# Kernel tuning notes

Hardware: AMD Instinct MI355X
Metric: run time of the kernel (lower is better)

Reference implementation:

```python
import jax, jax.numpy as jnp
import numpy as np

HEAD_DIM = 128
PROJ_DIM = 64


def setup_inputs() -> dict:
    key = jax.random.key(0)
    kq, kk, kv, kr = jax.random.split(key, 4)
    B, H, NQ, NKV = 1, 16, 2048, 4096
    Q = jax.random.normal(kq, (B, H, NQ, HEAD_DIM), dtype=jnp.float32)
    K = jax.random.normal(kk, (B, H, NKV, HEAD_DIM), dtype=jnp.float32)
    V = jax.random.normal(kv, (B, H, NKV, HEAD_DIM), dtype=jnp.float32)
    # R ~ N(0,1) / sqrt(proj_dim), as in the torch __init__
    R = jax.random.normal(kr, (HEAD_DIM, PROJ_DIM), dtype=jnp.float32) / (PROJ_DIM ** 0.5)
    return {"Q": Q, "K": K, "V": V, "R": R}


def reference(Q, K, V, R):
    proj_dim = R.shape[-1]
    scale = 1.0 / (proj_dim ** 0.5)
    # Project Q and K into the random-projection space: [B,H,N,proj_dim]
    Q_proj = jnp.einsum('bhnd,dp->bhnp', Q, R)
    K_proj = jnp.einsum('bhmd,dp->bhmp', K, R)
    # scores: [B,H,NQ,NKV]
    scores = jnp.einsum('bhnp,bhmp->bhnm', Q_proj, K_proj) * scale
    weights = jax.nn.softmax(scores, axis=-1)
    # output: [B,H,NQ,head_dim]
    return jnp.einsum('bhnm,bhmd->bhnd', weights, V)
```

## Files before the change

kernel.cpp:

```cpp
#include <hip/hip_runtime.h>

#define HEADS 16
#define NQ    2048
#define NKV   4096
#define DH    128
#define PDIM  64

typedef __bf16 bf16_t;
typedef bf16_t bf16x8 __attribute__((ext_vector_type(8)));
typedef float  f32x4  __attribute__((ext_vector_type(4)));

__global__ __launch_bounds__(256) void proj_kernel(
    const float* __restrict__ Q, const float* __restrict__ K,
    const float* __restrict__ R, bf16_t* __restrict__ Qp, bf16_t* __restrict__ Kp)
{
  const int tid  = threadIdx.x;
  const int wave = tid >> 6, lane = tid & 63;
  const int n16  = lane & 15, quad = lane >> 4;

  bf16x8 bfr[4][4];
#pragma unroll
  for (int nt = 0; nt < 4; ++nt) {
    const int n = nt * 16 + n16;
#pragma unroll
    for (int kk = 0; kk < 4; ++kk) {
      const int k0 = kk * 32 + quad * 8;
      bf16x8 b;
#pragma unroll
      for (int j = 0; j < 8; ++j) b[j] = (bf16_t)R[(k0 + j) * PDIM + n];
      bfr[nt][kk] = b;
    }
  }

  const long rowblock = (long)blockIdx.x * 256 + wave * 64;
  const long qrows = (long)HEADS * NQ;

#pragma unroll 1
  for (int t = 0; t < 4; ++t) {
    const long r0 = rowblock + t * 16;
    const float* X; bf16_t* Y; float scale; long xrow;
    if (r0 < qrows) { X = Q; Y = Qp; scale = 0.18033688011112042f; xrow = r0; }
    else            { X = K; Y = Kp; scale = 1.0f;                 xrow = r0 - qrows; }

    const float* xp = X + (xrow + n16) * DH;
    bf16x8 a[4];
#pragma unroll
    for (int kk = 0; kk < 4; ++kk) {
      const int k0 = kk * 32 + quad * 8;
      f32x4 x0 = *(const f32x4*)(xp + k0);
      f32x4 x1 = *(const f32x4*)(xp + k0 + 4);
      bf16x8 av;
#pragma unroll
      for (int j = 0; j < 4; ++j) { av[j] = (bf16_t)(x0[j] * scale); av[4 + j] = (bf16_t)(x1[j] * scale); }
      a[kk] = av;
    }
#pragma unroll
    for (int nt = 0; nt < 4; ++nt) {
      f32x4 acc = {0.f, 0.f, 0.f, 0.f};
#pragma unroll
      for (int kk = 0; kk < 4; ++kk)
        acc = __builtin_amdgcn_mfma_f32_16x16x32_bf16(a[kk], bfr[nt][kk], acc, 0, 0, 0);
#pragma unroll
      for (int r = 0; r < 4; ++r)
        Y[(xrow + quad * 4 + r) * PDIM + nt * 16 + n16] = (bf16_t)acc[r];
    }
  }
}

__global__ __launch_bounds__(256) void vtrans_kernel(
    const float* __restrict__ V, bf16_t* __restrict__ Vt)
{
  __shared__ float sF[64 * 129];
  const int tid = threadIdx.x;
  const int h = blockIdx.y, jt = blockIdx.x;
  const float* vp = V + ((long)h * NKV + jt * 64) * DH;
#pragma unroll
  for (int rep = 0; rep < 8; ++rep) {
    const int slot = tid + rep * 256;
    const int j = slot >> 5, c4 = (slot & 31) * 4;
    f32x4 v = *(const f32x4*)(vp + j * DH + c4);
    float* dst = &sF[j * 129 + c4];
    dst[0] = v[0]; dst[1] = v[1]; dst[2] = v[2]; dst[3] = v[3];
  }
  __syncthreads();
  bf16_t* op = Vt + (long)h * DH * NKV + jt * 64;
#pragma unroll
  for (int rep = 0; rep < 4; ++rep) {
    const int slot = tid + rep * 256;
    const int d = slot >> 3, j8 = (slot & 7) * 8;
    bf16x8 w;
#pragma unroll
    for (int jj = 0; jj < 8; ++jj) w[jj] = (bf16_t)sF[(j8 + jj) * 129 + d];
    *(bf16x8*)(op + (long)d * NKV + j8) = w;
  }
}

__global__ __launch_bounds__(128, 2) void flash_kernel(
    const bf16_t* __restrict__ Qp, const bf16_t* __restrict__ Kp,
    const bf16_t* __restrict__ Vt, float* __restrict__ Out)
{
  const int tid  = threadIdx.x;
  const int wave = tid >> 6, lane = tid & 63;
  const int n16  = lane & 15, quad = lane >> 4;

  const int h  = blockIdx.x & 15;
  const int qt = blockIdx.x >> 4;

  __shared__ bf16_t sK[64 * 72];
  __shared__ bf16_t sV[128 * 72];
  __shared__ bf16_t sP[2][32 * 72];

  bf16x8 aq[2][2];
#pragma unroll
  for (int mh = 0; mh < 2; ++mh) {
    const bf16_t* qrow = Qp + ((long)h * NQ + qt * 64 + wave * 32 + mh * 16 + n16) * PDIM;
    aq[mh][0] = *(const bf16x8*)(qrow + quad * 8);
    aq[mh][1] = *(const bf16x8*)(qrow + 32 + quad * 8);
  }

  f32x4 o[2][8];
  float rsum[2][4];
  const f32x4 zero = {0.f, 0.f, 0.f, 0.f};
#pragma unroll
  for (int mh = 0; mh < 2; ++mh) {
#pragma unroll
    for (int d = 0; d < 8; ++d) o[mh][d] = zero;
#pragma unroll
    for (int r = 0; r < 4; ++r) rsum[mh][r] = 0.f;
  }

  const bf16_t* kpH = Kp + (long)h * NKV * PDIM;
  const bf16_t* vtH = Vt + (long)h * DH * NKV;

  for (int t = 0; t < NKV / 64; ++t) {
    __syncthreads();
    {
      const bf16_t* src = kpH + t * (64 * PDIM);
#pragma unroll
      for (int rep = 0; rep < 4; ++rep) {
        const int slot = tid + rep * 128;
        const int row = slot >> 3, c8 = (slot & 7) * 8;
        *(bf16x8*)(&sK[row * 72 + c8]) = *(const bf16x8*)(src + row * 64 + c8);
      }
      const bf16_t* vsrc = vtH + t * 64;
#pragma unroll
      for (int rep = 0; rep < 8; ++rep) {
        const int slot = tid + rep * 128;
        const int row = slot >> 3, c8 = (slot & 7) * 8;
        *(bf16x8*)(&sV[row * 72 + c8]) = *(const bf16x8*)(vsrc + (long)row * NKV + c8);
      }
    }
    __syncthreads();

    f32x4 s[2][4];
#pragma unroll
    for (int nt = 0; nt < 4; ++nt) {
      const bf16_t* kb = &sK[(nt * 16 + n16) * 72 + quad * 8];
      const bf16x8 b0 = *(const bf16x8*)(kb);
      const bf16x8 b1 = *(const bf16x8*)(kb + 32);
#pragma unroll
      for (int mh = 0; mh < 2; ++mh) {
        f32x4 acc = __builtin_amdgcn_mfma_f32_16x16x32_bf16(aq[mh][0], b0, zero, 0, 0, 0);
        s[mh][nt]  = __builtin_amdgcn_mfma_f32_16x16x32_bf16(aq[mh][1], b1, acc, 0, 0, 0);
      }
    }

    bf16_t* pw = sP[wave];
#pragma unroll
    for (int mh = 0; mh < 2; ++mh) {
#pragma unroll
      for (int nt = 0; nt < 4; ++nt) {
#pragma unroll
        for (int r = 0; r < 4; ++r) {
          const float p = __builtin_amdgcn_exp2f(s[mh][nt][r]);
          rsum[mh][r] += p;
          pw[(mh * 16 + quad * 4 + r) * 72 + nt * 16 + n16] = (bf16_t)p;
        }
      }
    }

    bf16x8 ap[2][2];
#pragma unroll
    for (int mh = 0; mh < 2; ++mh) {
      const bf16_t* pr = &pw[(mh * 16 + n16) * 72];
      ap[mh][0] = *(const bf16x8*)(pr + quad * 8);
      ap[mh][1] = *(const bf16x8*)(pr + 32 + quad * 8);
    }
#pragma unroll
    for (int dt = 0; dt < 8; ++dt) {
      const bf16_t* vb = &sV[(dt * 16 + n16) * 72 + quad * 8];
      const bf16x8 b0 = *(const bf16x8*)(vb);
      const bf16x8 b1 = *(const bf16x8*)(vb + 32);
#pragma unroll
      for (int mh = 0; mh < 2; ++mh) {
        o[mh][dt] = __builtin_amdgcn_mfma_f32_16x16x32_bf16(ap[mh][0], b0, o[mh][dt], 0, 0, 0);
        o[mh][dt] = __builtin_amdgcn_mfma_f32_16x16x32_bf16(ap[mh][1], b1, o[mh][dt], 0, 0, 0);
      }
    }
  }

#pragma unroll
  for (int mh = 0; mh < 2; ++mh) {
    float inv[4];
#pragma unroll
    for (int r = 0; r < 4; ++r) {
      float v = rsum[mh][r];
      v += __shfl_xor(v, 1, 16);
      v += __shfl_xor(v, 2, 16);
      v += __shfl_xor(v, 4, 16);
      v += __shfl_xor(v, 8, 16);
      inv[r] = 1.f / v;
    }
    float* ob = Out + ((long)h * NQ + qt * 64 + wave * 32 + mh * 16 + quad * 4) * DH + n16;
#pragma unroll
    for (int dt = 0; dt < 8; ++dt)
#pragma unroll
      for (int r = 0; r < 4; ++r)
        ob[(long)r * DH + dt * 16] = o[mh][dt][r] * inv[r];
  }
}

extern "C" void kernel_launch(void* const* d_in, const int* in_sizes, int n_in,
                              void* d_out, int out_size, void* d_ws, size_t ws_size,
                              hipStream_t stream)
{
  const float* Q = (const float*)d_in[0];
  const float* K = (const float*)d_in[1];
  const float* V = (const float*)d_in[2];
  const float* R = (const float*)d_in[3];
  float* Out = (float*)d_out;

  char* ws = (char*)d_ws;
  bf16_t* Qp = (bf16_t*)(ws);
  bf16_t* Kp = (bf16_t*)(ws + (size_t)(4  << 20));
  bf16_t* Vt = (bf16_t*)(ws + (size_t)(12 << 20));

  proj_kernel<<<384, 256, 0, stream>>>(Q, K, R, Qp, Kp);
  vtrans_kernel<<<dim3(64, 16), 256, 0, stream>>>(V, Vt);
  flash_kernel<<<512, 128, 0, stream>>>(Qp, Kp, Vt, Out);
}
```

Before: 228.8 us.

## Split KV across blocks with combine pass, enlarge Q tile, coalesce projection stores

```diff
diff --git a/kernel.cpp b/kernel.cpp
--- a/kernel.cpp
+++ b/kernel.cpp
@@ -8,12 +8,14 @@
 
 typedef __bf16 bf16_t;
 typedef bf16_t bf16x8 __attribute__((ext_vector_type(8)));
+typedef bf16_t bf16x4 __attribute__((ext_vector_type(4)));
 typedef float  f32x4  __attribute__((ext_vector_type(4)));
 
 __global__ __launch_bounds__(256) void proj_kernel(
     const float* __restrict__ Q, const float* __restrict__ K,
     const float* __restrict__ R, bf16_t* __restrict__ Qp, bf16_t* __restrict__ Kp)
 {
+  __shared__ bf16_t sY[4][16 * 72];
   const int tid  = threadIdx.x;
   const int wave = tid >> 6, lane = tid & 63;
   const int n16  = lane & 15, quad = lane >> 4;
@@ -54,6 +56,7 @@
       for (int j = 0; j < 4; ++j) { av[j] = (bf16_t)(x0[j] * scale); av[4 + j] = (bf16_t)(x1[j] * scale); }
       a[kk] = av;
     }
+    bf16_t* sy = sY[wave];
 #pragma unroll
     for (int nt = 0; nt < 4; ++nt) {
       f32x4 acc = {0.f, 0.f, 0.f, 0.f};
@@ -62,8 +65,13 @@
         acc = __builtin_amdgcn_mfma_f32_16x16x32_bf16(a[kk], bfr[nt][kk], acc, 0, 0, 0);
 #pragma unroll
       for (int r = 0; r < 4; ++r)
-        Y[(xrow + quad * 4 + r) * PDIM + nt * 16 + n16] = (bf16_t)acc[r];
-    }
+        sy[(quad * 4 + r) * 72 + nt * 16 + n16] = (bf16_t)acc[r];
+    }
+    const int row = lane >> 2, cg = lane & 3;
+    bf16x8 w0 = *(const bf16x8*)(&sy[row * 72 + cg * 16]);
+    bf16x8 w1 = *(const bf16x8*)(&sy[row * 72 + cg * 16 + 8]);
+    *(bf16x8*)(Y + (xrow + row) * PDIM + cg * 16)     = w0;
+    *(bf16x8*)(Y + (xrow + row) * PDIM + cg * 16 + 8) = w1;
   }
 }
 
@@ -97,52 +105,58 @@
 
 __global__ __launch_bounds__(128, 2) void flash_kernel(
     const bf16_t* __restrict__ Qp, const bf16_t* __restrict__ Kp,
-    const bf16_t* __restrict__ Vt, float* __restrict__ Out)
+    const bf16_t* __restrict__ Vt, bf16_t* __restrict__ Opart,
+    float* __restrict__ Lpart, float* __restrict__ Out,
+    int splits, int iters)
 {
   const int tid  = threadIdx.x;
   const int wave = tid >> 6, lane = tid & 63;
   const int n16  = lane & 15, quad = lane >> 4;
 
   const int h  = blockIdx.x & 15;
-  const int qt = blockIdx.x >> 4;
+  const int qt = (blockIdx.x >> 4) & 15;
+  const int sp = blockIdx.x >> 8;
+
+  const int qbase = qt * 128 + wave * 64;
+  const int kv0   = sp * (64 * iters);
 
   __shared__ bf16_t sK[64 * 72];
   __shared__ bf16_t sV[128 * 72];
-  __shared__ bf16_t sP[2][32 * 72];
-
-  bf16x8 aq[2][2];
-#pragma unroll
-  for (int mh = 0; mh < 2; ++mh) {
-    const bf16_t* qrow = Qp + ((long)h * NQ + qt * 64 + wave * 32 + mh * 16 + n16) * PDIM;
-    aq[mh][0] = *(const bf16x8*)(qrow + quad * 8);
-    aq[mh][1] = *(const bf16x8*)(qrow + 32 + quad * 8);
-  }
-
-  f32x4 o[2][8];
-  float rsum[2][4];
+  __shared__ bf16_t sP[2][64 * 72];
+
+  bf16x8 qf[4][2];
+#pragma unroll
+  for (int g = 0; g < 4; ++g) {
+    const bf16_t* qr = Qp + ((long)h * NQ + qbase + g * 16 + n16) * PDIM;
+    qf[g][0] = *(const bf16x8*)(qr + quad * 8);
+    qf[g][1] = *(const bf16x8*)(qr + 32 + quad * 8);
+  }
+
+  f32x4 o[4][8];
+  float rsum[4];
   const f32x4 zero = {0.f, 0.f, 0.f, 0.f};
 #pragma unroll
-  for (int mh = 0; mh < 2; ++mh) {
-#pragma unroll
-    for (int d = 0; d < 8; ++d) o[mh][d] = zero;
-#pragma unroll
-    for (int r = 0; r < 4; ++r) rsum[mh][r] = 0.f;
+  for (int g = 0; g < 4; ++g) {
+    rsum[g] = 0.f;
+#pragma unroll
+    for (int d = 0; d < 8; ++d) o[g][d] = zero;
   }
 
   const bf16_t* kpH = Kp + (long)h * NKV * PDIM;
   const bf16_t* vtH = Vt + (long)h * DH * NKV;
-
-  for (int t = 0; t < NKV / 64; ++t) {
+  bf16_t* pw = sP[wave];
+
+  for (int t = 0; t < iters; ++t) {
     __syncthreads();
     {
-      const bf16_t* src = kpH + t * (64 * PDIM);
+      const bf16_t* src = kpH + (long)(kv0 + t * 64) * PDIM;
 #pragma unroll
       for (int rep = 0; rep < 4; ++rep) {
         const int slot = tid + rep * 128;
         const int row = slot >> 3, c8 = (slot & 7) * 8;
         *(bf16x8*)(&sK[row * 72 + c8]) = *(const bf16x8*)(src + row * 64 + c8);
       }
-      const bf16_t* vsrc = vtH + t * 64;
+      const bf16_t* vsrc = vtH + kv0 + t * 64;
 #pragma unroll
       for (int rep = 0; rep < 8; ++rep) {
         const int slot = tid + rep * 128;
@@ -152,39 +166,31 @@
     }
     __syncthreads();
 
-    f32x4 s[2][4];
-#pragma unroll
-    for (int nt = 0; nt < 4; ++nt) {
-      const bf16_t* kb = &sK[(nt * 16 + n16) * 72 + quad * 8];
-      const bf16x8 b0 = *(const bf16x8*)(kb);
-      const bf16x8 b1 = *(const bf16x8*)(kb + 32);
-#pragma unroll
-      for (int mh = 0; mh < 2; ++mh) {
-        f32x4 acc = __builtin_amdgcn_mfma_f32_16x16x32_bf16(aq[mh][0], b0, zero, 0, 0, 0);
-        s[mh][nt]  = __builtin_amdgcn_mfma_f32_16x16x32_bf16(aq[mh][1], b1, acc, 0, 0, 0);
-      }
-    }
-
-    bf16_t* pw = sP[wave];
-#pragma unroll
-    for (int mh = 0; mh < 2; ++mh) {
-#pragma unroll
-      for (int nt = 0; nt < 4; ++nt) {
-#pragma unroll
-        for (int r = 0; r < 4; ++r) {
-          const float p = __builtin_amdgcn_exp2f(s[mh][nt][r]);
-          rsum[mh][r] += p;
-          pw[(mh * 16 + quad * 4 + r) * 72 + nt * 16 + n16] = (bf16_t)p;
-        }
-      }
-    }
-
-    bf16x8 ap[2][2];
-#pragma unroll
-    for (int mh = 0; mh < 2; ++mh) {
-      const bf16_t* pr = &pw[(mh * 16 + n16) * 72];
-      ap[mh][0] = *(const bf16x8*)(pr + quad * 8);
-      ap[mh][1] = *(const bf16x8*)(pr + 32 + quad * 8);
+#pragma unroll
+    for (int mt = 0; mt < 4; ++mt) {
+      const bf16_t* ka = &sK[(mt * 16 + n16) * 72 + quad * 8];
+      const bf16x8 a0 = *(const bf16x8*)(ka);
+      const bf16x8 a1 = *(const bf16x8*)(ka + 32);
+#pragma unroll
+      for (int g = 0; g < 4; ++g) {
+        f32x4 s = __builtin_amdgcn_mfma_f32_16x16x32_bf16(a0, qf[g][0], zero, 0, 0, 0);
+        s       = __builtin_amdgcn_mfma_f32_16x16x32_bf16(a1, qf[g][1], s,    0, 0, 0);
+        float p0 = __builtin_amdgcn_exp2f(s[0]);
+        float p1 = __builtin_amdgcn_exp2f(s[1]);
+        float p2 = __builtin_amdgcn_exp2f(s[2]);
+        float p3 = __builtin_amdgcn_exp2f(s[3]);
+        rsum[g] += (p0 + p1) + (p2 + p3);
+        bf16x4 pk = { (bf16_t)p0, (bf16_t)p1, (bf16_t)p2, (bf16_t)p3 };
+        *(bf16x4*)(&pw[(g * 16 + n16) * 72 + mt * 16 + quad * 4]) = pk;
+      }
+    }
+
+    bf16x8 ap[4][2];
+#pragma unroll
+    for (int g = 0; g < 4; ++g) {
+      const bf16_t* pr = &pw[(g * 16 + n16) * 72];
+      ap[g][0] = *(const bf16x8*)(pr + quad * 8);
+      ap[g][1] = *(const bf16x8*)(pr + 32 + quad * 8);
     }
 #pragma unroll
     for (int dt = 0; dt < 8; ++dt) {
@@ -192,32 +198,76 @@
       const bf16x8 b0 = *(const bf16x8*)(vb);
       const bf16x8 b1 = *(const bf16x8*)(vb + 32);
 #pragma unroll
-      for (int mh = 0; mh < 2; ++mh) {
-        o[mh][dt] = __builtin_amdgcn_mfma_f32_16x16x32_bf16(ap[mh][0], b0, o[mh][dt], 0, 0, 0);
-        o[mh][dt] = __builtin_amdgcn_mfma_f32_16x16x32_bf16(ap[mh][1], b1, o[mh][dt], 0, 0, 0);
-      }
-    }
-  }
-
-#pragma unroll
-  for (int mh = 0; mh < 2; ++mh) {
-    float inv[4];
-#pragma unroll
-    for (int r = 0; r < 4; ++r) {
-      float v = rsum[mh][r];
-      v += __shfl_xor(v, 1, 16);
-      v += __shfl_xor(v, 2, 16);
-      v += __shfl_xor(v, 4, 16);
-      v += __shfl_xor(v, 8, 16);
-      inv[r] = 1.f / v;
-    }
-    float* ob = Out + ((long)h * NQ + qt * 64 + wave * 32 + mh * 16 + quad * 4) * DH + n16;
-#pragma unroll
-    for (int dt = 0; dt < 8; ++dt)
-#pragma unroll
-      for (int r = 0; r < 4; ++r)
-        ob[(long)r * DH + dt * 16] = o[mh][dt][r] * inv[r];
-  }
+      for (int g = 0; g < 4; ++g) {
+        o[g][dt] = __builtin_amdgcn_mfma_f32_16x16x32_bf16(ap[g][0], b0, o[g][dt], 0, 0, 0);
+        o[g][dt] = __builtin_amdgcn_mfma_f32_16x16x32_bf16(ap[g][1], b1, o[g][dt], 0, 0, 0);
+      }
+    }
+  }
+
+  float lsum[4];
+#pragma unroll
+  for (int g = 0; g < 4; ++g) {
+    float v = rsum[g];
+    v += __shfl_xor(v, 16);
+    v += __shfl_xor(v, 32);
+    lsum[g] = v;
+  }
+
+  if (splits > 1) {
+    if (quad == 0) {
+#pragma unroll
+      for (int g = 0; g < 4; ++g)
+        Lpart[((long)sp * HEADS + h) * NQ + qbase + g * 16 + n16] = lsum[g];
+    }
+    bf16_t* ob = Opart + (((long)sp * HEADS + h) * NQ + qbase) * DH;
+#pragma unroll
+    for (int g = 0; g < 4; ++g)
+#pragma unroll
+      for (int dt = 0; dt < 8; ++dt)
+#pragma unroll
+        for (int r = 0; r < 4; ++r)
+          ob[(long)(g * 16 + quad * 4 + r) * DH + dt * 16 + n16] = (bf16_t)o[g][dt][r];
+  } else {
+    float* ob = Out + ((long)h * NQ + qbase) * DH;
+#pragma unroll
+    for (int g = 0; g < 4; ++g) {
+      const float inv = 1.f / lsum[g];
+#pragma unroll
+      for (int r = 0; r < 4; ++r) {
+        const float rinv = __shfl(inv, quad * 4 + r, 16);
+#pragma unroll
+        for (int dt = 0; dt < 8; ++dt)
+          ob[(long)(g * 16 + quad * 4 + r) * DH + dt * 16 + n16] = o[g][dt][r] * rinv;
+      }
+    }
+  }
+}
+
+__global__ __launch_bounds__(256) void combine_kernel(
+    const bf16_t* __restrict__ Opart, const float* __restrict__ Lpart,
+    float* __restrict__ Out)
+{
+  const long idx = (long)blockIdx.x * 256 + threadIdx.x;
+  const int  d8  = (int)(idx & 15);
+  const long hq  = idx >> 4;
+  float l = 0.f;
+  float acc[8];
+#pragma unroll
+  for (int j = 0; j < 8; ++j) acc[j] = 0.f;
+#pragma unroll
+  for (int s = 0; s < 4; ++s) {
+    l += Lpart[s * (long)(HEADS * NQ) + hq];
+    bf16x8 v = *(const bf16x8*)(Opart + (s * (long)(HEADS * NQ) + hq) * DH + d8 * 8);
+#pragma unroll
+    for (int j = 0; j < 8; ++j) acc[j] += (float)v[j];
+  }
+  const float inv = 1.f / l;
+  f32x4 o0 = { acc[0] * inv, acc[1] * inv, acc[2] * inv, acc[3] * inv };
+  f32x4 o1 = { acc[4] * inv, acc[5] * inv, acc[6] * inv, acc[7] * inv };
+  float* op = Out + hq * DH + d8 * 8;
+  *(f32x4*)(op)     = o0;
+  *(f32x4*)(op + 4) = o1;
 }
 
 extern "C" void kernel_launch(void* const* d_in, const int* in_sizes, int n_in,
@@ -234,8 +284,17 @@
   bf16_t* Qp = (bf16_t*)(ws);
   bf16_t* Kp = (bf16_t*)(ws + (size_t)(4  << 20));
   bf16_t* Vt = (bf16_t*)(ws + (size_t)(12 << 20));
+  bf16_t* Opart = (bf16_t*)(ws + (size_t)(28 << 20));
+  float*  Lpart = (float*)(ws + (size_t)(60 << 20));
+
+  const size_t need4 = (size_t)(60 << 20) + 4ull * HEADS * NQ * sizeof(float);
+  const int splits = (ws_size >= need4) ? 4 : 1;
+  const int iters  = NKV / (64 * splits);
 
   proj_kernel<<<384, 256, 0, stream>>>(Q, K, R, Qp, Kp);
   vtrans_kernel<<<dim3(64, 16), 256, 0, stream>>>(V, Vt);
-  flash_kernel<<<512, 128, 0, stream>>>(Qp, Kp, Vt, Out);
-}
+  flash_kernel<<<splits * 256, 128, 0, stream>>>(Qp, Kp, Vt, Opart, Lpart, Out,
+                                                 splits, iters);
+  if (splits == 4)
+    combine_kernel<<<2048, 256, 0, stream>>>(Opart, Lpart, Out);
+}
```

Measured after the change: 338.4 us. 47.9% more time.
